# Kernel optimization log

Measured on AMD Instinct MI355X. Metric: run time of the kernel, lower is better.

The kernel has to match this reference:

```python
import jax, jax.numpy as jnp
import numpy as np

N = 131072   # nodes
C = 64       # in_channels
K = 32       # n_super_nodes
B = 16       # graphs in batch
EPS = 1e-9
TAU = 1.0


def setup_inputs() -> dict:
    key = jax.random.key(0)
    ks = jax.random.split(key, 8)
    x = jax.random.normal(ks[0], (N, C), dtype=jnp.float32)
    batch = jnp.sort(jax.random.randint(ks[1], (N,), 0, B)).astype(jnp.int32)
    pos = jax.random.normal(ks[2], (N, 2), dtype=jnp.float32)
    u = jax.random.uniform(ks[3], (N, K), dtype=jnp.float32)  # uniform noise for gumbel
    W1 = jax.random.normal(ks[4], (C, C), dtype=jnp.float32) / jnp.sqrt(C)
    b1 = jnp.zeros((C,), dtype=jnp.float32)
    W2 = jax.random.normal(ks[5], (C, K), dtype=jnp.float32) / jnp.sqrt(C)
    b2 = jnp.zeros((K,), dtype=jnp.float32)
    scaling = jnp.ones((1,), dtype=jnp.float32)
    active_mask = jnp.ones((K,), dtype=jnp.float32)
    return {"x": x, "batch": batch, "pos": pos, "u": u, "W1": W1, "b1": b1,
            "W2": W2, "b2": b2, "scaling": scaling, "active_mask": active_mask}


def reference(x, batch, pos, u, W1, b1, W2, b2, scaling, active_mask):
    # assignment MLP: Linear -> ReLU -> Linear, then learned scaling
    logits = (jax.nn.relu(x @ W1 + b1) @ W2 + b2) * scaling[0]  # [N, K]
    # eval-mode masking of inactive super-nodes
    logits = jnp.where(active_mask[None, :] == 0, -1e9, logits)
    # gumbel-softmax (soft, hard=False)
    g = -jnp.log(-jnp.log(u + EPS) + EPS)
    s = jax.nn.softmax((logits + g) / TAU, axis=-1)           # [N, K]

    avg_s = s.mean(axis=0)                                     # [K]
    entropy = -jnp.mean(jnp.sum(s * jnp.log(s + EPS), axis=1))
    diversity = jnp.sum(avg_s * jnp.log(avg_s + EPS))
    pruning = jnp.mean(jnp.abs(avg_s * (1.0 - active_mask)))
    sparsity = jnp.sum(active_mask) / K

    # global spatial variance of each super-node cluster
    s_sum = s.sum(axis=0, keepdims=True) + EPS                 # [1, K]
    s_norm = s / s_sum                                         # [N, K]
    mu_g = s_norm.T @ pos                                      # [K, 2]
    pos_sq = jnp.sum(pos ** 2, axis=1, keepdims=True)          # [N, 1]
    var = (s_norm.T @ pos_sq)[:, 0] - 2.0 * jnp.sum(mu_g * (s_norm.T @ pos), axis=1) \
          + jnp.sum(mu_g ** 2, axis=1)                         # [K]
    spatial = var.mean()

    # per-graph super-node centroids via scatter-sum over batch index
    sum_s_pos = jax.ops.segment_sum(pos[:, None, :] * s[:, :, None], batch,
                                    num_segments=B)            # [B, K, 2]
    sum_s = jax.ops.segment_sum(s, batch, num_segments=B)[..., None] + EPS  # [B, K, 1]
    mu = sum_s_pos / sum_s                                     # [B, K, 2]

    # pairwise separation (repulsion) among super-node centroids
    dist_sq = jnp.sum((mu[:, :, None, :] - mu[:, None, :, :]) ** 2, axis=-1)  # [B, K, K]
    eye = jnp.eye(K, dtype=mu.dtype)[None]
    separation = jnp.sum((1.0 / (dist_sq + 1.0)) * (1.0 - eye)) / (K * (K - 1) + EPS)

    # pooled features: outer product then scatter-sum  ->  [B, K, C]
    out = jax.ops.segment_sum(x[:, None, :] * s[:, :, None], batch, num_segments=B)

    return (out, s, entropy, diversity, spatial, pruning, sparsity, separation, mu)
```

## Files before the change

kernel.cpp:

```cpp
#include <hip/hip_runtime.h>

#define EPS 1e-9f
constexpr int NN = 131072;
constexpr int CD = 64;
constexpr int KK = 32;
constexpr int BB = 16;

constexpr int WS_ENT  = 0;
constexpr int WS_BACC = 16;
constexpr int FP      = 72;
constexpr int WS_BACC_SZ = BB * KK * FP;
constexpr int WS_TAG  = WS_BACC + WS_BACC_SZ;
constexpr int WS_PART = WS_TAG + 1040;
constexpr int CELLS   = 68 * 32;

constexpr int OUT_OUT  = 0;
constexpr int OUT_S    = BB * KK * CD;
constexpr int OUT_SCAL = OUT_S + NN * KK;
constexpr int OUT_MU   = OUT_SCAL + 6;

__global__ __launch_bounds__(256, 4)
void node_k(const float* __restrict__ x,
            const float* __restrict__ u,
            const float* __restrict__ W1,
            const float* __restrict__ b1,
            const float* __restrict__ W2,
            const float* __restrict__ b2,
            const float* __restrict__ scaling,
            const float* __restrict__ amask,
            float* __restrict__ s_out,
            float* __restrict__ ent_acc) {
    const int n = blockIdx.x * 256 + threadIdx.x;
    const float* xr = x + (size_t)n * 64;
    float logit[32];
#pragma unroll
    for (int k = 0; k < 32; k++) logit[k] = b2[k];

    for (int jb = 0; jb < 4; jb++) {
        float h[16];
#pragma unroll
        for (int jj = 0; jj < 16; jj++) h[jj] = b1[jb * 16 + jj];
#pragma unroll
        for (int c4 = 0; c4 < 16; c4++) {
            const float4 xq = *(const float4*)(xr + c4 * 4);
            const float xs4[4] = {xq.x, xq.y, xq.z, xq.w};
#pragma unroll
            for (int q = 0; q < 4; q++) {
                const float xc = xs4[q];
                const float* w1r = W1 + (c4 * 4 + q) * 64 + jb * 16;
#pragma unroll
                for (int jj = 0; jj < 16; jj++)
                    h[jj] = fmaf(xc, w1r[jj], h[jj]);
            }
        }
#pragma unroll
        for (int jj = 0; jj < 16; jj++) {
            const float hj = fmaxf(h[jj], 0.f);
            const float* w2r = W2 + (jb * 16 + jj) * 32;
#pragma unroll
            for (int k = 0; k < 32; k++)
                logit[k] = fmaf(hj, w2r[k], logit[k]);
        }
    }

    const float sc = scaling[0];
    const float* ur = u + (size_t)n * 32;
    float m = -3.0e38f;
#pragma unroll
    for (int k4 = 0; k4 < 8; k4++) {
        float4 uv = *(const float4*)(ur + 4 * k4);
        float us[4] = {uv.x, uv.y, uv.z, uv.w};
#pragma unroll
        for (int q = 0; q < 4; q++) {
            const int k = 4 * k4 + q;
            float l = logit[k] * sc;
            l = (amask[k] == 0.f) ? -1e9f : l;
            float g = -__logf(-__logf(us[q] + EPS) + EPS);
            float z = l + g;
            logit[k] = z;
            m = fmaxf(m, z);
        }
    }
    float e0 = 0.f, e1 = 0.f, e2 = 0.f, e3 = 0.f;
#pragma unroll
    for (int k = 0; k < 32; k += 4) {
        float a = __expf(logit[k] - m);     logit[k] = a;     e0 += a;
        float b = __expf(logit[k + 1] - m); logit[k + 1] = b; e1 += b;
        float c = __expf(logit[k + 2] - m); logit[k + 2] = c; e2 += c;
        float d = __expf(logit[k + 3] - m); logit[k + 3] = d; e3 += d;
    }
    const float inv = 1.f / ((e0 + e1) + (e2 + e3));
    float ent = 0.f;
#pragma unroll
    for (int k = 0; k < 32; k++) {
        float sv = logit[k] * inv;
        logit[k] = sv;
        ent += sv * __logf(sv + EPS);
    }
    float* so = s_out + (size_t)n * 32;
#pragma unroll
    for (int k4 = 0; k4 < 8; k4++)
        *(float4*)(so + 4 * k4) = make_float4(logit[4 * k4], logit[4 * k4 + 1],
                                              logit[4 * k4 + 2], logit[4 * k4 + 3]);
#pragma unroll
    for (int off = 32; off > 0; off >>= 1) ent += __shfl_down(ent, off, 64);
    if ((threadIdx.x & 63) == 0) atomicAdd(ent_acc, ent);
}

__global__ void pool_k(const float* __restrict__ s,
                       const float* __restrict__ x,
                       const float* __restrict__ pos,
                       const int* __restrict__ batch,
                       float* __restrict__ bacc,
                       float* __restrict__ part,
                       int* __restrict__ tags,
                       int npb) {
    const int t = threadIdx.x;
    const int k = t & 31;
    const int fg = t >> 5;
    const int base = blockIdx.x * npb;
    float acc[8];
    float accx = 0.f;
#pragma unroll
    for (int f = 0; f < 8; f++) acc[f] = 0.f;
    int cur_b = batch[base];
#pragma unroll 2
    for (int n = base; n < base + npb; n++) {
        const int b = batch[n];
        if (b != cur_b) {
            float* dst = bacc + (cur_b * 32 + k) * FP;
#pragma unroll
            for (int f = 0; f < 8; f++) { atomicAdd(dst + fg * 8 + f, acc[f]); acc[f] = 0.f; }
            if (fg < 4) { atomicAdd(dst + 64 + fg, accx); accx = 0.f; }
            cur_b = b;
        }
        const float sv = s[n * 32 + k];
        const float4 v0 = *(const float4*)(x + n * 64 + fg * 8);
        const float4 v1 = *(const float4*)(x + n * 64 + fg * 8 + 4);
        acc[0] = fmaf(sv, v0.x, acc[0]);
        acc[1] = fmaf(sv, v0.y, acc[1]);
        acc[2] = fmaf(sv, v0.z, acc[2]);
        acc[3] = fmaf(sv, v0.w, acc[3]);
        acc[4] = fmaf(sv, v1.x, acc[4]);
        acc[5] = fmaf(sv, v1.y, acc[5]);
        acc[6] = fmaf(sv, v1.z, acc[6]);
        acc[7] = fmaf(sv, v1.w, acc[7]);
        if (fg < 4) {
            float2 p = *(const float2*)(pos + n * 2);
            float e = (fg == 0) ? p.x : (fg == 1) ? p.y
                    : (fg == 2) ? (p.x * p.x + p.y * p.y) : 1.f;
            accx = fmaf(sv, e, accx);
        }
    }
    float* pp = part + (size_t)blockIdx.x * CELLS;
#pragma unroll
    for (int f = 0; f < 8; f++) pp[(fg * 8 + f) * 32 + k] = acc[f];
    if (fg < 4) pp[(64 + fg) * 32 + k] = accx;
    if (t == 0) tags[blockIdx.x] = cur_b;
}

__global__ void reduce_k(const float* __restrict__ part,
                         const int* __restrict__ tags,
                         float* __restrict__ bacc,
                         float* __restrict__ outp,
                         int nblk) {
    const int b = blockIdx.x;
    const int cell = blockIdx.y * 256 + threadIdx.x;
    if (cell >= CELLS) return;
    const int k = cell & 31, f = cell >> 5;
    int lo = 0, hi = nblk;
    while (lo < hi) { int mid = (lo + hi) >> 1; if (tags[mid] < b) lo = mid + 1; else hi = mid; }
    int lo2 = lo, hi2 = nblk;
    while (lo2 < hi2) { int mid = (lo2 + hi2) >> 1; if (tags[mid] < b + 1) lo2 = mid + 1; else hi2 = mid; }
    float v = 0.f;
    for (int blk = lo; blk < lo2; blk++)
        v += part[(size_t)blk * CELLS + cell];
    const int idx = (b * 32 + k) * FP + f;
    const float tot = bacc[idx] + v;
    bacc[idx] = tot;
    if (f < 64) outp[OUT_OUT + ((b * 32 + k) << 6) + f] = tot;
}

__global__ void fin_k(const float* __restrict__ ws,
                      const float* __restrict__ amask,
                      float* __restrict__ outp) {
    const int t = threadIdx.x;
    const float* bacc = ws + WS_BACC;
    __shared__ float mu_s[BB * KK * 2];
    for (int idx = t; idx < BB * KK * 2; idx += 256) {
        int bk = idx >> 1, d = idx & 1;
        float v = bacc[bk * FP + 64 + d] / (bacc[bk * FP + 67] + EPS);
        mu_s[idx] = v;
        outp[OUT_MU + idx] = v;
    }
    __shared__ float kred[32][4];
    if (t < 32) {
        float S = 0, px = 0, py = 0, sq = 0;
        for (int b = 0; b < 16; b++) {
            const float* pp = bacc + (b * 32 + t) * FP;
            S += pp[67]; px += pp[64]; py += pp[65]; sq += pp[66];
        }
        float avg = S / (float)NN;
        float am = amask[t];
        float ssum = S + EPS;
        float mx = px / ssum, my = py / ssum;
        kred[t][0] = avg * __logf(avg + EPS);
        kred[t][1] = fabsf(avg * (1.f - am));
        kred[t][2] = sq / ssum - mx * mx - my * my;
        kred[t][3] = am;
    }
    __syncthreads();
    float sep = 0.f;
    for (int idx = t; idx < BB * KK * KK; idx += 256) {
        int b = idx >> 10, i = (idx >> 5) & 31, j = idx & 31;
        if (i != j) {
            float dx = mu_s[(b * 32 + i) * 2 + 0] - mu_s[(b * 32 + j) * 2 + 0];
            float dy = mu_s[(b * 32 + i) * 2 + 1] - mu_s[(b * 32 + j) * 2 + 1];
            sep += 1.f / (dx * dx + dy * dy + 1.f);
        }
    }
    __shared__ float red[256];
    red[t] = sep;
    __syncthreads();
    for (int s2 = 128; s2 > 0; s2 >>= 1) {
        if (t < s2) red[t] += red[t + s2];
        __syncthreads();
    }
    if (t == 0) {
        float div = 0, pru = 0, spa = 0, spar = 0;
        for (int kq = 0; kq < 32; kq++) {
            div += kred[kq][0]; pru += kred[kq][1];
            spa += kred[kq][2]; spar += kred[kq][3];
        }
        outp[OUT_SCAL + 0] = -ws[WS_ENT] / (float)NN;
        outp[OUT_SCAL + 1] = div;
        outp[OUT_SCAL + 2] = spa / 32.f;
        outp[OUT_SCAL + 3] = pru / 32.f;
        outp[OUT_SCAL + 4] = spar / 32.f;
        outp[OUT_SCAL + 5] = red[0] / (32.f * 31.f + EPS);
    }
}

extern "C" void kernel_launch(void* const* d_in, const int* in_sizes, int n_in,
                              void* d_out, int out_size, void* d_ws, size_t ws_size,
                              hipStream_t stream) {
    const float* x       = (const float*)d_in[0];
    const int*   batch   = (const int*)d_in[1];
    const float* pos     = (const float*)d_in[2];
    const float* u       = (const float*)d_in[3];
    const float* W1      = (const float*)d_in[4];
    const float* b1      = (const float*)d_in[5];
    const float* W2      = (const float*)d_in[6];
    const float* b2      = (const float*)d_in[7];
    const float* scaling = (const float*)d_in[8];
    const float* amask   = (const float*)d_in[9];
    float* outp = (float*)d_out;
    float* ws   = (float*)d_ws;

    int npb = 128;
    while (npb < NN &&
           ws_size < ((size_t)WS_PART + (size_t)(NN / npb) * CELLS) * sizeof(float))
        npb <<= 1;
    const int nblk = NN / npb;

    hipMemsetAsync(ws, 0, (size_t)(WS_BACC + WS_BACC_SZ) * sizeof(float), stream);
    node_k<<<NN / 256, 256, 0, stream>>>(x, u, W1, b1, W2, b2, scaling, amask,
                                         outp + OUT_S, ws + WS_ENT);
    pool_k<<<nblk, 256, 0, stream>>>(outp + OUT_S, x, pos, batch,
                                     ws + WS_BACC, ws + WS_PART, (int*)(ws + WS_TAG), npb);
    reduce_k<<<dim3(BB, (CELLS + 255) / 256), 256, 0, stream>>>(
        ws + WS_PART, (const int*)(ws + WS_TAG), ws + WS_BACC, outp, nblk);
    fin_k<<<1, 256, 0, stream>>>(ws, amask, outp);
}
```

Baseline: 246.0 us.

## Compute assignment MLP with bf16 MFMA and split softmax across four lanes

Replaces the per-thread scalar FP32 MLP with bf16 MFMA 16x16x32 tiles. A small prep kernel pre-packs W1 and W2 (with scaling folded in) into fragment layout and folds the mask and scaling into b2. Hidden activations pass through swizzled LDS, and logits go to LDS so four threads share each node's softmax, with shuffles for the max and sum reductions. Entropy atomics drop to one per block. This cuts the FMA-bound cost of the MLP, but bf16 rounding of x, W and hidden values changes the logits and may exceed tolerance.

```diff
diff --git a/kernel.cpp b/kernel.cpp
--- a/kernel.cpp
+++ b/kernel.cpp
@@ -6,12 +6,18 @@
 constexpr int KK = 32;
 constexpr int BB = 16;
 
+typedef __attribute__((ext_vector_type(8))) short short8;
+typedef __attribute__((ext_vector_type(4))) float f32x4;
+
 constexpr int WS_ENT  = 0;
 constexpr int WS_BACC = 16;
 constexpr int FP      = 72;
 constexpr int WS_BACC_SZ = BB * KK * FP;
-constexpr int WS_TAG  = WS_BACC + WS_BACC_SZ;
-constexpr int WS_PART = WS_TAG + 1040;
+constexpr int WS_W1F  = WS_BACC + WS_BACC_SZ;
+constexpr int WS_W2F  = WS_W1F + 2048;
+constexpr int WS_B2F  = WS_W2F + 1024;
+constexpr int WS_TAG  = WS_B2F + 32;
+constexpr int WS_PART = 41024;
 constexpr int CELLS   = 68 * 32;
 
 constexpr int OUT_OUT  = 0;
@@ -19,92 +25,140 @@
 constexpr int OUT_SCAL = OUT_S + NN * KK;
 constexpr int OUT_MU   = OUT_SCAL + 6;
 
-__global__ __launch_bounds__(256, 4)
-void node_k(const float* __restrict__ x,
-            const float* __restrict__ u,
-            const float* __restrict__ W1,
-            const float* __restrict__ b1,
-            const float* __restrict__ W2,
-            const float* __restrict__ b2,
-            const float* __restrict__ scaling,
-            const float* __restrict__ amask,
-            float* __restrict__ s_out,
-            float* __restrict__ ent_acc) {
-    const int n = blockIdx.x * 256 + threadIdx.x;
-    const float* xr = x + (size_t)n * 64;
-    float logit[32];
-#pragma unroll
-    for (int k = 0; k < 32; k++) logit[k] = b2[k];
-
-    for (int jb = 0; jb < 4; jb++) {
-        float h[16];
-#pragma unroll
-        for (int jj = 0; jj < 16; jj++) h[jj] = b1[jb * 16 + jj];
-#pragma unroll
-        for (int c4 = 0; c4 < 16; c4++) {
-            const float4 xq = *(const float4*)(xr + c4 * 4);
-            const float xs4[4] = {xq.x, xq.y, xq.z, xq.w};
-#pragma unroll
-            for (int q = 0; q < 4; q++) {
-                const float xc = xs4[q];
-                const float* w1r = W1 + (c4 * 4 + q) * 64 + jb * 16;
-#pragma unroll
-                for (int jj = 0; jj < 16; jj++)
-                    h[jj] = fmaf(xc, w1r[jj], h[jj]);
-            }
-        }
-#pragma unroll
-        for (int jj = 0; jj < 16; jj++) {
-            const float hj = fmaxf(h[jj], 0.f);
-            const float* w2r = W2 + (jb * 16 + jj) * 32;
-#pragma unroll
-            for (int k = 0; k < 32; k++)
-                logit[k] = fmaf(hj, w2r[k], logit[k]);
-        }
-    }
-
+__device__ __forceinline__ unsigned short f2bf(float f) {
+    unsigned b = __builtin_bit_cast(unsigned, f);
+    b += 0x7fffu + ((b >> 16) & 1u);
+    return (unsigned short)(b >> 16);
+}
+
+__global__ void prep_k(const float* __restrict__ W1, const float* __restrict__ W2,
+                       const float* __restrict__ b2, const float* __restrict__ scaling,
+                       const float* __restrict__ amask, float* __restrict__ ws) {
+    const int t = threadIdx.x;
     const float sc = scaling[0];
-    const float* ur = u + (size_t)n * 32;
+    unsigned short* w1f = (unsigned short*)(ws + WS_W1F);
+    for (int idx = t; idx < 4096; idx += 256) {
+        int e = idx & 7, lane = (idx >> 3) & 63, f = idx >> 9;
+        int nt = f >> 1, ks = f & 1;
+        int j = nt * 16 + (lane & 15);
+        int c = ks * 32 + (lane >> 4) * 8 + e;
+        w1f[idx] = f2bf(W1[c * 64 + j]);
+    }
+    unsigned short* w2f = (unsigned short*)(ws + WS_W2F);
+    for (int idx = t; idx < 2048; idx += 256) {
+        int e = idx & 7, lane = (idx >> 3) & 63, f = idx >> 9;
+        int nt = f >> 1, ks = f & 1;
+        int j = nt * 16 + (lane & 15);
+        int c = ks * 32 + (lane >> 4) * 8 + e;
+        w2f[idx] = f2bf(sc * W2[c * 32 + j]);
+    }
+    if (t < 32) ws[WS_B2F + t] = (amask[t] == 0.f) ? -1e9f : b2[t] * sc;
+}
+
+__global__ __launch_bounds__(256)
+void node_k(const float* __restrict__ x, const float* __restrict__ u,
+            const float* __restrict__ b1, const float* __restrict__ ws,
+            float* __restrict__ s_out, float* __restrict__ ent_acc) {
+    __shared__ unsigned short Hlds[4096];
+    __shared__ float Llds[64 * 33];
+    __shared__ float entred[4];
+    const int t = threadIdx.x;
+    const int w = t >> 6, l = t & 63, lj = l & 15, lg = l >> 4;
+    const unsigned short* w1f = (const unsigned short*)(ws + WS_W1F);
+    const unsigned short* w2f = (const unsigned short*)(ws + WS_W2F);
+    const float* b2f = ws + WS_B2F;
+
+    const int node = blockIdx.x * 64 + w * 16 + lj;
+    const float* xr = x + (size_t)node * 64 + lg * 8;
+    short8 a0, a1;
+    {
+        float4 p0 = *(const float4*)xr;
+        float4 p1 = *(const float4*)(xr + 4);
+        float4 p2 = *(const float4*)(xr + 32);
+        float4 p3 = *(const float4*)(xr + 36);
+        a0[0] = f2bf(p0.x); a0[1] = f2bf(p0.y); a0[2] = f2bf(p0.z); a0[3] = f2bf(p0.w);
+        a0[4] = f2bf(p1.x); a0[5] = f2bf(p1.y); a0[6] = f2bf(p1.z); a0[7] = f2bf(p1.w);
+        a1[0] = f2bf(p2.x); a1[1] = f2bf(p2.y); a1[2] = f2bf(p2.z); a1[3] = f2bf(p2.w);
+        a1[4] = f2bf(p3.x); a1[5] = f2bf(p3.y); a1[6] = f2bf(p3.z); a1[7] = f2bf(p3.w);
+    }
+    f32x4 hacc[4];
+#pragma unroll
+    for (int nt = 0; nt < 4; nt++) {
+        f32x4 acc = {0.f, 0.f, 0.f, 0.f};
+        short8 b0 = *(const short8*)(w1f + (nt * 2 + 0) * 512 + l * 8);
+        short8 b1v = *(const short8*)(w1f + (nt * 2 + 1) * 512 + l * 8);
+        acc = __builtin_amdgcn_mfma_f32_16x16x32_bf16(a0, b0, acc, 0, 0, 0);
+        acc = __builtin_amdgcn_mfma_f32_16x16x32_bf16(a1, b1v, acc, 0, 0, 0);
+        hacc[nt] = acc;
+    }
+#pragma unroll
+    for (int nt = 0; nt < 4; nt++) {
+        const float bias = b1[nt * 16 + lj];
+#pragma unroll
+        for (int q = 0; q < 4; q++) {
+            const int r = lg * 4 + q;
+            const float hv = fmaxf(hacc[nt][q] + bias, 0.f);
+            const int bo = (nt * 32 + lj * 2) ^ ((r & 7) << 4);
+            Hlds[w * 1024 + r * 64 + (bo >> 1)] = f2bf(hv);
+        }
+    }
+    short8 a20, a21;
+    {
+        const int base = w * 1024 + lj * 64;
+        a20 = *(const short8*)(Hlds + base + ((lg ^ (lj & 7)) << 3));
+        a21 = *(const short8*)(Hlds + base + (((4 + lg) ^ (lj & 7)) << 3));
+    }
+#pragma unroll
+    for (int nt = 0; nt < 2; nt++) {
+        f32x4 acc = {0.f, 0.f, 0.f, 0.f};
+        short8 b0 = *(const short8*)(w2f + (nt * 2 + 0) * 512 + l * 8);
+        short8 b1v = *(const short8*)(w2f + (nt * 2 + 1) * 512 + l * 8);
+        acc = __builtin_amdgcn_mfma_f32_16x16x32_bf16(a20, b0, acc, 0, 0, 0);
+        acc = __builtin_amdgcn_mfma_f32_16x16x32_bf16(a21, b1v, acc, 0, 0, 0);
+        const float bb = b2f[nt * 16 + lj];
+#pragma unroll
+        for (int q = 0; q < 4; q++)
+            Llds[(w * 16 + lg * 4 + q) * 33 + nt * 16 + lj] = acc[q] + bb;
+    }
+    __syncthreads();
+
+    const int nl = t >> 2, sub = t & 3;
+    const int n = blockIdx.x * 64 + nl;
+    const float* Lr = &Llds[nl * 33 + sub * 8];
+    const float* ur = u + (size_t)n * 32 + sub * 8;
+    float4 u0 = *(const float4*)ur, u1 = *(const float4*)(ur + 4);
+    float uu[8] = {u0.x, u0.y, u0.z, u0.w, u1.x, u1.y, u1.z, u1.w};
+    float z[8];
     float m = -3.0e38f;
 #pragma unroll
-    for (int k4 = 0; k4 < 8; k4++) {
-        float4 uv = *(const float4*)(ur + 4 * k4);
-        float us[4] = {uv.x, uv.y, uv.z, uv.w};
-#pragma unroll
-        for (int q = 0; q < 4; q++) {
-            const int k = 4 * k4 + q;
-            float l = logit[k] * sc;
-            l = (amask[k] == 0.f) ? -1e9f : l;
-            float g = -__logf(-__logf(us[q] + EPS) + EPS);
-            float z = l + g;
-            logit[k] = z;
-            m = fmaxf(m, z);
-        }
-    }
-    float e0 = 0.f, e1 = 0.f, e2 = 0.f, e3 = 0.f;
-#pragma unroll
-    for (int k = 0; k < 32; k += 4) {
-        float a = __expf(logit[k] - m);     logit[k] = a;     e0 += a;
-        float b = __expf(logit[k + 1] - m); logit[k + 1] = b; e1 += b;
-        float c = __expf(logit[k + 2] - m); logit[k + 2] = c; e2 += c;
-        float d = __expf(logit[k + 3] - m); logit[k + 3] = d; e3 += d;
-    }
-    const float inv = 1.f / ((e0 + e1) + (e2 + e3));
+    for (int i = 0; i < 8; i++) {
+        float g = -__logf(-__logf(uu[i] + EPS) + EPS);
+        z[i] = Lr[i] + g;
+        m = fmaxf(m, z[i]);
+    }
+    m = fmaxf(m, __shfl_xor(m, 1, 64));
+    m = fmaxf(m, __shfl_xor(m, 2, 64));
+    float es = 0.f;
+#pragma unroll
+    for (int i = 0; i < 8; i++) { z[i] = __expf(z[i] - m); es += z[i]; }
+    es += __shfl_xor(es, 1, 64);
+    es += __shfl_xor(es, 2, 64);
+    const float inv = 1.f / es;
     float ent = 0.f;
 #pragma unroll
-    for (int k = 0; k < 32; k++) {
-        float sv = logit[k] * inv;
-        logit[k] = sv;
+    for (int i = 0; i < 8; i++) {
+        float sv = z[i] * inv;
+        z[i] = sv;
         ent += sv * __logf(sv + EPS);
     }
-    float* so = s_out + (size_t)n * 32;
-#pragma unroll
-    for (int k4 = 0; k4 < 8; k4++)
-        *(float4*)(so + 4 * k4) = make_float4(logit[4 * k4], logit[4 * k4 + 1],
-                                              logit[4 * k4 + 2], logit[4 * k4 + 3]);
+    float* so = s_out + (size_t)n * 32 + sub * 8;
+    *(float4*)so = make_float4(z[0], z[1], z[2], z[3]);
+    *(float4*)(so + 4) = make_float4(z[4], z[5], z[6], z[7]);
 #pragma unroll
     for (int off = 32; off > 0; off >>= 1) ent += __shfl_down(ent, off, 64);
-    if ((threadIdx.x & 63) == 0) atomicAdd(ent_acc, ent);
+    if (l == 0) entred[w] = ent;
+    __syncthreads();
+    if (t == 0) atomicAdd(ent_acc, entred[0] + entred[1] + entred[2] + entred[3]);
 }
 
 __global__ void pool_k(const float* __restrict__ s,
@@ -264,8 +318,8 @@
     const int nblk = NN / npb;
 
     hipMemsetAsync(ws, 0, (size_t)(WS_BACC + WS_BACC_SZ) * sizeof(float), stream);
-    node_k<<<NN / 256, 256, 0, stream>>>(x, u, W1, b1, W2, b2, scaling, amask,
-                                         outp + OUT_S, ws + WS_ENT);
+    prep_k<<<1, 256, 0, stream>>>(W1, W2, b2, scaling, amask, ws);
+    node_k<<<NN / 64, 256, 0, stream>>>(x, u, b1, ws, outp + OUT_S, ws + WS_ENT);
     pool_k<<<nblk, 256, 0, stream>>>(outp + OUT_S, x, pos, batch,
                                      ws + WS_BACC, ws + WS_PART, (int*)(ws + WS_TAG), npb);
     reduce_k<<<dim3(BB, (CELLS + 255) / 256), 256, 0, stream>>>(
```

Result: faster. 220.0 us (-10.6%).
